# Performance work log

Measured on AMD Instinct MI355X. Metric: run time of the kernel, lower is better.

Reference implementation:

```python
import jax, jax.numpy as jnp
import numpy as np

N, E, IN, H, C, ED = 50000, 800000, 128, 4, 64, 4
NEG_SLOPE = 0.2


def setup_inputs() -> dict:
    key = jax.random.key(0)
    ks = iter(jax.random.split(key, 40))
    def p(shape, s=0.05):
        return jax.random.normal(next(ks), shape, jnp.float32) * s
    inp = dict(
        x=jax.random.normal(next(ks), (N, IN), jnp.float32),
        edge_index=jax.random.randint(next(ks), (2, E), 0, N),
        edge_attr=jax.random.normal(next(ks), (E, ED), jnp.float32),
        # GATConv layer 1 (concat=True)
        W1=p((IN, H * C)), att_src1=p((H, C)), att_dst1=p((H, C)),
        We1=p((ED, H * C)), att_e1=p((H, C)), b1=p((H * C,)),
        g1=jnp.ones((H * C,), jnp.float32), be1=jnp.zeros((H * C,), jnp.float32),
        # GATConv layer 2 (concat=False -> mean over heads)
        W2=p((H * C, H * C)), att_src2=p((H, C)), att_dst2=p((H, C)),
        We2=p((ED, H * C)), att_e2=p((H, C)), b2=p((C,)),
        g2=jnp.ones((C,), jnp.float32), be2=jnp.zeros((C,), jnp.float32),
        # skip / MLP head
        skip_W=p((IN, C)), skip_b=p((C,)),
        fc1_W=p((C, C // 2)), fc1_b=p((C // 2,)),
        fc2_W=p((C // 2, 1)), fc2_b=p((1,)),
    )
    return inp


def _add_self_loops(edge_index, edge_attr, n):
    # PyG GATConv default: add_self_loops=True, fill_value='mean'
    src, dst = edge_index[0], edge_index[1]
    sums = jax.ops.segment_sum(edge_attr, dst, num_segments=n)
    cnt = jax.ops.segment_sum(jnp.ones((edge_attr.shape[0], 1), edge_attr.dtype), dst, num_segments=n)
    mean_attr = sums / jnp.maximum(cnt, 1.0)
    loop = jnp.arange(n)
    src = jnp.concatenate([src, loop])
    dst = jnp.concatenate([dst, loop])
    ea = jnp.concatenate([edge_attr, mean_attr], axis=0)
    return src, dst, ea


def _gat_layer(x, src, dst, ea, W, a_src, a_dst, We, a_e, bias, n, concat):
    xs = (x @ W).reshape(n, H, C)                     # [N,H,C]
    alpha_src = (xs * a_src).sum(-1)                  # [N,H]
    alpha_dst = (xs * a_dst).sum(-1)                  # [N,H]
    ep = (ea @ We).reshape(-1, H, C)                  # [Et,H,C]
    alpha_e = (ep * a_e).sum(-1)                      # [Et,H]
    alpha = jax.nn.leaky_relu(alpha_src[src] + alpha_dst[dst] + alpha_e, NEG_SLOPE)
    # segment softmax over destination nodes
    m = jax.ops.segment_max(alpha, dst, num_segments=n)
    alpha = jnp.exp(alpha - m[dst])
    denom = jax.ops.segment_sum(alpha, dst, num_segments=n)
    alpha = alpha / (denom[dst] + 1e-16)
    out = jax.ops.segment_sum(xs[src] * alpha[:, :, None], dst, num_segments=n)  # [N,H,C]
    out = out.reshape(n, H * C) if concat else out.mean(axis=1)
    return out + bias


def _bn(x, g, b):
    mu = x.mean(0)
    var = x.var(0)
    return (x - mu) * jax.lax.rsqrt(var + 1e-5) * g + b


def reference(x, edge_index, edge_attr, W1, att_src1, att_dst1, We1, att_e1, b1, g1, be1,
              W2, att_src2, att_dst2, We2, att_e2, b2, g2, be2,
              skip_W, skip_b, fc1_W, fc1_b, fc2_W, fc2_b):
    n = x.shape[0]
    src, dst, ea = _add_self_loops(edge_index, edge_attr, n)
    residual = x @ skip_W + skip_b
    h = _gat_layer(x, src, dst, ea, W1, att_src1, att_dst1, We1, att_e1, b1, n, True)
    h = jax.nn.elu(_bn(h, g1, be1))
    h = _gat_layer(h, src, dst, ea, W2, att_src2, att_dst2, We2, att_e2, b2, n, False)
    h = jax.nn.elu(_bn(h, g2, be2))
    h = h + residual
    h = jax.nn.relu(h @ fc1_W + fc1_b)
    h = jax.nn.softplus(h @ fc2_W + fc2_b)
    return h.squeeze(-1)
```

## Files before the change

kernel.cpp:

```cpp
#include <hip/hip_runtime.h>
#include <math.h>

static constexpr int N_NODES = 50000;
static constexpr int N_EDGES = 800000;
static constexpr int IN_F = 128;
static constexpr int CH = 64;
static constexpr int HC = 256;
static constexpr float NEG_SLOPE = 0.2f;

typedef __attribute__((ext_vector_type(8))) short bf16x8;
typedef __attribute__((ext_vector_type(4))) float f32x4;

__device__ __forceinline__ unsigned pack_bf(float a, float b) {
    unsigned ua = __float_as_uint(a) + 0x8000u;
    unsigned ub = __float_as_uint(b) + 0x8000u;
    return __builtin_amdgcn_perm(ub, ua, 0x07060302u);
}
__device__ __forceinline__ float bflo(unsigned u) { return __uint_as_float(u << 16); }
__device__ __forceinline__ float bfhi(unsigned u) { return __uint_as_float(u & 0xffff0000u); }
__device__ __forceinline__ float bfs(unsigned short u) {
    return __uint_as_float((unsigned)u << 16);
}
__device__ __forceinline__ float elu(float v) { return v > 0.f ? v : __expf(v) - 1.0f; }

__device__ __forceinline__ int sigma(int p) { return ((p & 15) << 4) | (p >> 4); }

static constexpr int EB_BLK = (N_EDGES + 255) / 256;
static constexpr int CONV_ITEMS = 106496 + 32;
static constexpr int CONV_BLK = (CONV_ITEMS + 255) / 256;
static constexpr int GEMM_BLKS = (N_NODES + 63) / 64;

__global__ void hist_conv(const int* __restrict__ ei, int* __restrict__ deg,
                          const float* __restrict__ W1, const float* __restrict__ W2,
                          const float* __restrict__ Ws, const float* __restrict__ We1,
                          const float* __restrict__ atte1, const float* __restrict__ We2,
                          const float* __restrict__ atte2, unsigned short* __restrict__ WT1,
                          unsigned short* __restrict__ WT2, unsigned short* __restrict__ WTs,
                          float* __restrict__ weff) {
    if (blockIdx.x < EB_BLK) {
        int e = blockIdx.x * 256 + threadIdx.x;
        if (e < N_EDGES) atomicAdd(&deg[ei[N_EDGES + e]], 1);
        return;
    }
    int t = (blockIdx.x - EB_BLK) * 256 + threadIdx.x;
    if (t < 32768) {
        int k = t >> 8, n = t & 255;
        unsigned u = __float_as_uint(W1[t]) + 0x8000u;
        WT1[n * 128 + k] = (unsigned short)(u >> 16);
    } else if (t < 98304) {
        int u2 = t - 32768;
        int k = u2 >> 8, n = u2 & 255;
        unsigned u = __float_as_uint(W2[u2]) + 0x8000u;
        WT2[n * 256 + sigma(k)] = (unsigned short)(u >> 16);
    } else if (t < 106496) {
        int u2 = t - 98304;
        int k = u2 >> 6, n = u2 & 63;
        unsigned u = __float_as_uint(Ws[u2]) + 0x8000u;
        WTs[n * 128 + k] = (unsigned short)(u >> 16);
    } else if (t < 106496 + 32) {
        int idx = t - 106496;
        const float* We = idx < 16 ? We1 : We2;
        const float* ae = idx < 16 ? atte1 : atte2;
        int j = idx & 15;
        int d = j >> 2, h = j & 3;
        float s = 0.f;
        for (int c = 0; c < CH; ++c) s += We[d * HC + h * CH + c] * ae[h * CH + c];
        weff[idx] = s;
    }
}

__global__ void scan_block(const int* __restrict__ deg, int* __restrict__ rowptr,
                           int* __restrict__ bsum) {
    __shared__ int s[256];
    int tid = threadIdx.x;
    int i = blockIdx.x * 256 + tid;
    int v = (i < N_NODES) ? deg[i] : 0;
    s[tid] = v;
    __syncthreads();
    for (int off = 1; off < 256; off <<= 1) {
        int t = (tid >= off) ? s[tid - off] : 0;
        __syncthreads();
        s[tid] += t;
        __syncthreads();
    }
    if (i < N_NODES) rowptr[i] = s[tid] - v;
    if (tid == 255) bsum[blockIdx.x] = s[255];
}

__global__ void scan_add2(int* __restrict__ rowptr, const int* __restrict__ bsum,
                          int* __restrict__ fillc, int nb) {
    __shared__ int s[256];
    int tid = threadIdx.x;
    int v = (tid < nb) ? bsum[tid] : 0;
    s[tid] = v;
    __syncthreads();
    for (int off = 1; off < 256; off <<= 1) {
        int t = (tid >= off) ? s[tid - off] : 0;
        __syncthreads();
        s[tid] += t;
        __syncthreads();
    }
    int boff = (blockIdx.x == 0) ? 0 : s[blockIdx.x - 1];
    int i = blockIdx.x * 256 + tid;
    if (i < N_NODES) {
        rowptr[i] += boff;
        fillc[i] = 0;
    }
    if (i == N_NODES) rowptr[N_NODES] = N_EDGES;
}

template <int K, bool ABF, bool BN, bool SKIP, bool FILL>
__global__ __launch_bounds__(256) void gemm_mfma_att(
    const void* __restrict__ Av, const unsigned short* __restrict__ BT,
    const float* __restrict__ colsum, const float* __restrict__ g,
    const float* __restrict__ be, float invM,
    const unsigned short* __restrict__ BTs, const float* __restrict__ skip_b,
    float* __restrict__ residual,
    const float* __restrict__ att_src, const float* __restrict__ att_dst,
    unsigned short* __restrict__ xsb, float* __restrict__ asrc, float* __restrict__ adst,
    int M, const int* __restrict__ ei, const float4* __restrict__ ea,
    const int* __restrict__ rowptr, int* __restrict__ fillc, uint4* __restrict__ edrec) {
    if constexpr (FILL) {
        if (blockIdx.x >= GEMM_BLKS) {
            int e = (blockIdx.x - GEMM_BLKS) * 256 + threadIdx.x;
            if (e < N_EDGES) {
                int s = ei[e];
                int t = ei[N_EDGES + e];
                const float4 v = ea[e];
                int p = atomicAdd(&fillc[t], 1);
                edrec[rowptr[t] + p] =
                    make_uint4((unsigned)s, (unsigned)t, pack_bf(v.x, v.y), pack_bf(v.z, v.w));
            }
            return;
        }
    }
    constexpr int NT = 16;
    __shared__ float s_scale[256], s_shift[256];
    if constexpr (BN) {
        int c = threadIdx.x;
        int tc = sigma(c);
        float mean = colsum[c] * invM;
        float var = colsum[256 + c] * invM - mean * mean;
        float sc = g[tc] * rsqrtf(var + 1e-5f);
        s_scale[c] = sc;
        s_shift[c] = be[tc] - mean * sc;
        __syncthreads();
    }
    const int lane = threadIdx.x & 63;
    const int wid = threadIdx.x >> 6;
    const int r0 = blockIdx.x * 64 + wid * 16;
    const int lr = lane & 15;
    const int kg = lane >> 4;
    f32x4 acc[NT] = {};
    f32x4 accS[4] = {};
    const float* af = (const float*)Av;
    const unsigned short* ab = (const unsigned short*)Av;
    int rr = r0 + lr;
    if (rr >= M) rr = M - 1;
    const size_t rowoff = (size_t)rr * K + kg * 8;
    const unsigned short* brow = BT + (size_t)lr * K + kg * 8;
    const unsigned short* brow_s = SKIP ? BTs + (size_t)lr * K + kg * 8 : nullptr;
    for (int k0 = 0; k0 < K; k0 += 32) {
        float4 sc0, sc1, sh0, sh1;
        if constexpr (BN) {
            sc0 = *reinterpret_cast<const float4*>(&s_scale[k0 + kg * 8]);
            sc1 = *reinterpret_cast<const float4*>(&s_scale[k0 + kg * 8 + 4]);
            sh0 = *reinterpret_cast<const float4*>(&s_shift[k0 + kg * 8]);
            sh1 = *reinterpret_cast<const float4*>(&s_shift[k0 + kg * 8 + 4]);
        }
        bf16x8 a;
        if constexpr (!ABF) {
            const float4 lo = *reinterpret_cast<const float4*>(af + rowoff + k0);
            const float4 hi = *reinterpret_cast<const float4*>(af + rowoff + k0 + 4);
            union { bf16x8 v; unsigned u[4]; } fa;
            fa.u[0] = pack_bf(lo.x, lo.y);
            fa.u[1] = pack_bf(lo.z, lo.w);
            fa.u[2] = pack_bf(hi.x, hi.y);
            fa.u[3] = pack_bf(hi.z, hi.w);
            a = fa.v;
        } else {
            union { bf16x8 v; unsigned short us[8]; unsigned u[4]; } fa;
            fa.v = *reinterpret_cast<const bf16x8*>(ab + rowoff + k0);
            if constexpr (BN) {
                float f0 = elu(fmaf(bfs(fa.us[0]), sc0.x, sh0.x));
                float f1 = elu(fmaf(bfs(fa.us[1]), sc0.y, sh0.y));
                float f2 = elu(fmaf(bfs(fa.us[2]), sc0.z, sh0.z));
                float f3 = elu(fmaf(bfs(fa.us[3]), sc0.w, sh0.w));
                float f4 = elu(fmaf(bfs(fa.us[4]), sc1.x, sh1.x));
                float f5 = elu(fmaf(bfs(fa.us[5]), sc1.y, sh1.y));
                float f6 = elu(fmaf(bfs(fa.us[6]), sc1.z, sh1.z));
                float f7 = elu(fmaf(bfs(fa.us[7]), sc1.w, sh1.w));
                fa.u[0] = pack_bf(f0, f1);
                fa.u[1] = pack_bf(f2, f3);
                fa.u[2] = pack_bf(f4, f5);
                fa.u[3] = pack_bf(f6, f7);
            }
            a = fa.v;
        }
#pragma unroll
        for (int c = 0; c < NT; ++c) {
            bf16x8 b = *reinterpret_cast<const bf16x8*>(brow + (size_t)c * 16 * K + k0);
            acc[c] = __builtin_amdgcn_mfma_f32_16x16x32_bf16(a, b, acc[c], 0, 0, 0);
        }
        if constexpr (SKIP) {
#pragma unroll
            for (int c = 0; c < 4; ++c) {
                bf16x8 b = *reinterpret_cast<const bf16x8*>(brow_s + (size_t)c * 16 * K + k0);
                accS[c] = __builtin_amdgcn_mfma_f32_16x16x32_bf16(a, b, accS[c], 0, 0, 0);
            }
        }
    }
    float attS[NT], attD[NT];
#pragma unroll
    for (int c = 0; c < NT; ++c) {
        attS[c] = att_src[c * 16 + lr];
        attD[c] = att_dst[c * 16 + lr];
    }
#pragma unroll
    for (int j = 0; j < 4; ++j) {
        int row = r0 + kg * 4 + j;
        bool valid = row < M;
        uint4 ua, ub;
        ua.x = pack_bf(acc[0][j], acc[1][j]);
        ua.y = pack_bf(acc[2][j], acc[3][j]);
        ua.z = pack_bf(acc[4][j], acc[5][j]);
        ua.w = pack_bf(acc[6][j], acc[7][j]);
        ub.x = pack_bf(acc[8][j], acc[9][j]);
        ub.y = pack_bf(acc[10][j], acc[11][j]);
        ub.z = pack_bf(acc[12][j], acc[13][j]);
        ub.w = pack_bf(acc[14][j], acc[15][j]);
        if (valid) {
            uint4* dst = reinterpret_cast<uint4*>(xsb + (size_t)row * HC) + lr * 2;
            dst[0] = ua;
            dst[1] = ub;
        }
        if constexpr (SKIP) {
            if (valid) {
#pragma unroll
                for (int c = 0; c < 4; ++c) {
                    int col = c * 16 + lr;
                    residual[(size_t)row * CH + col] = accS[c][j] + skip_b[col];
                }
            }
        }
#pragma unroll
        for (int h = 0; h < 4; ++h) {
            float ps = acc[4 * h + 0][j] * attS[4 * h + 0] +
                       acc[4 * h + 1][j] * attS[4 * h + 1] +
                       acc[4 * h + 2][j] * attS[4 * h + 2] +
                       acc[4 * h + 3][j] * attS[4 * h + 3];
            float pd = acc[4 * h + 0][j] * attD[4 * h + 0] +
                       acc[4 * h + 1][j] * attD[4 * h + 1] +
                       acc[4 * h + 2][j] * attD[4 * h + 2] +
                       acc[4 * h + 3][j] * attD[4 * h + 3];
#pragma unroll
            for (int mk = 1; mk < 16; mk <<= 1) {
                ps += __shfl_xor(ps, mk);
                pd += __shfl_xor(pd, mk);
            }
            if (valid && lr == 0) {
                asrc[row * 4 + h] = ps;
                adst[row * 4 + h] = pd;
            }
        }
    }
}

__global__ __launch_bounds__(256) void edge_w(
    const uint4* __restrict__ edrec, const float* __restrict__ weff,
    const float4* __restrict__ asrcv, const float4* __restrict__ adstv,
    uint4* __restrict__ pw) {
    int i = blockIdx.x * 256 + threadIdx.x;
    if (i >= N_EDGES) return;
    const uint4 er = edrec[i];
    int s = (int)er.x;
    int t = (int)er.y;
    const float vx = bflo(er.z), vy = bfhi(er.z), vz = bflo(er.w), vw = bfhi(er.w);
    const float4 as4 = asrcv[s];
    const float4 ad4 = adstv[t];
    const float asl[4] = {as4.x, as4.y, as4.z, as4.w};
    const float adl[4] = {ad4.x, ad4.y, ad4.z, ad4.w};
    float p[4], aev[4];
#pragma unroll
    for (int h = 0; h < 4; ++h) {
        float ae = vx * weff[h] + vy * weff[4 + h] + vz * weff[8 + h] + vw * weff[12 + h];
        float l = asl[h] + adl[h] + ae;
        l = fmaxf(l, NEG_SLOPE * l);
        p[h] = __expf(l);
        aev[h] = ae;
    }
    pw[i] = make_uint4(pack_bf(p[0], p[1]), pack_bf(p[2], p[3]),
                       pack_bf(aev[0], aev[1]), pack_bf(aev[2], aev[3]));
}

template <bool MEAN>
__global__ __launch_bounds__(256) void gat_node(
    const int* __restrict__ rowptr, const uint4* __restrict__ edrec,
    const uint4* __restrict__ pw, const float4* __restrict__ asrcv,
    const float4* __restrict__ adstv, const uint2* __restrict__ xsb,
    float* __restrict__ zbuf, void* __restrict__ outp) {
    if (blockIdx.x == 0) {
        zbuf[threadIdx.x] = 0.f;
        zbuf[256 + threadIdx.x] = 0.f;
    }
    int t = blockIdx.x * 4 + (threadIdx.x >> 6);
    if (t >= N_NODES) return;
    const int lane = threadIdx.x & 63;
    const int h = lane & 3;
    const unsigned sh = (h & 1) ? 0u : 16u;
    const bool hiW = (h & 2) != 0;
    const int start = rowptr[t], end = rowptr[t + 1];
    const int deg = end - start;
    const uint2* xl = xsb + lane;
    const unsigned* er32 = reinterpret_cast<const unsigned*>(edrec);
    float acc0 = 0.f, acc1 = 0.f, acc2 = 0.f, acc3 = 0.f;
    float psum = 0.f, aesum = 0.f;
    int i = start;
    for (; i + 8 <= end; i += 8) {
        uint2 f[8];
        float p[8], ae[8];
#pragma unroll
        for (int j = 0; j < 8; ++j) {
            int s = (int)er32[(size_t)(i + j) * 4];
            f[j] = xl[(size_t)s * 64];
            const uint4 w = pw[i + j];
            unsigned pword = hiW ? w.y : w.x;
            unsigned aeword = hiW ? w.w : w.z;
            p[j] = __uint_as_float((pword << sh) & 0xffff0000u);
            ae[j] = __uint_as_float((aeword << sh) & 0xffff0000u);
        }
#pragma unroll
        for (int j = 0; j < 8; ++j) {
            psum += p[j];
            aesum += ae[j];
            acc0 += bflo(f[j].x) * p[j];
            acc1 += bfhi(f[j].x) * p[j];
            acc2 += bflo(f[j].y) * p[j];
            acc3 += bfhi(f[j].y) * p[j];
        }
    }
    for (; i < end; ++i) {
        int s = (int)er32[(size_t)i * 4];
        uint2 f = xl[(size_t)s * 64];
        const uint4 w = pw[i];
        unsigned pword = hiW ? w.y : w.x;
        unsigned aeword = hiW ? w.w : w.z;
        float p = __uint_as_float((pword << sh) & 0xffff0000u);
        float ae = __uint_as_float((aeword << sh) & 0xffff0000u);
        psum += p;
        aesum += ae;
        acc0 += bflo(f.x) * p;
        acc1 += bfhi(f.x) * p;
        acc2 += bflo(f.y) * p;
        acc3 += bfhi(f.y) * p;
    }
    const float inv_deg = deg > 0 ? 1.0f / (float)deg : 1.0f;
    const float4 as4 = asrcv[t];
    const float4 ad4 = adstv[t];
    float asl = h == 0 ? as4.x : h == 1 ? as4.y : h == 2 ? as4.z : as4.w;
    float adl = h == 0 ? ad4.x : h == 1 ? ad4.y : h == 2 ? ad4.z : ad4.w;
    float l = asl + adl + aesum * inv_deg;
    l = fmaxf(l, NEG_SLOPE * l);
    const float pself = __expf(l);
    uint2 sf = xl[(size_t)t * 64];
    acc0 += bflo(sf.x) * pself;
    acc1 += bfhi(sf.x) * pself;
    acc2 += bflo(sf.y) * pself;
    acc3 += bfhi(sf.y) * pself;
    const float inv = 1.0f / (psum + pself + 1e-16f);
    acc0 *= inv; acc1 *= inv; acc2 *= inv; acc3 *= inv;
    if constexpr (MEAN) {
        acc0 += __shfl_xor(acc0, 1); acc0 += __shfl_xor(acc0, 2);
        acc1 += __shfl_xor(acc1, 1); acc1 += __shfl_xor(acc1, 2);
        acc2 += __shfl_xor(acc2, 1); acc2 += __shfl_xor(acc2, 2);
        acc3 += __shfl_xor(acc3, 1); acc3 += __shfl_xor(acc3, 2);
        if (h == 0) {
            int q = lane >> 2;
            float* o = reinterpret_cast<float*>(outp) + (size_t)t * CH + q;
            o[0] = 0.25f * acc0;
            o[16] = 0.25f * acc1;
            o[32] = 0.25f * acc2;
            o[48] = 0.25f * acc3;
        }
    } else {
        reinterpret_cast<uint2*>(outp)[(size_t)t * 64 + lane] =
            make_uint2(pack_bf(acc0, acc1), pack_bf(acc2, acc3));
    }
}

__global__ void colstats_bf(const unsigned short* __restrict__ X, float* __restrict__ sum,
                            float* __restrict__ sumsq, int M) {
    int c = threadIdx.x;
    int r0 = blockIdx.x * 256;
    int r1 = min(M, r0 + 256);
    float s = 0.f, q = 0.f;
    for (int r = r0; r < r1; ++r) {
        float v = bfs(X[(size_t)r * HC + c]);
        s += v;
        q += v * v;
    }
    atomicAdd(&sum[c], s);
    atomicAdd(&sumsq[c], q);
}

template <int F>
__global__ void colstats(const float* __restrict__ X, float* __restrict__ sum,
                         float* __restrict__ sumsq, int M) {
    const int NG = 256 / F;
    int c = threadIdx.x % F;
    int g = threadIdx.x / F;
    int r0 = blockIdx.x * 256;
    int r1 = min(M, r0 + 256);
    float s = 0.f, q = 0.f;
    for (int r = r0 + g; r < r1; r += NG) {
        float v = X[(size_t)r * F + c];
        s += v;
        q += v * v;
    }
    atomicAdd(&sum[c], s);
    atomicAdd(&sumsq[c], q);
}

__global__ __launch_bounds__(256) void head_mlp(
    const float* __restrict__ h2, const float* __restrict__ colsum,
    const float* __restrict__ g2, const float* __restrict__ be2, float invM,
    const float* __restrict__ residual, const float* __restrict__ fc1W,
    const float* __restrict__ fc1b, const float* __restrict__ fc2W,
    const float* __restrict__ fc2b, float* __restrict__ out) {
    __shared__ float s_sc[CH], s_sh[CH];
    if (threadIdx.x < CH) {
        int c = threadIdx.x;
        float mean = colsum[c] * invM;
        float var = colsum[256 + c] * invM - mean * mean;
        float sc = g2[c] * rsqrtf(var + 1e-5f);
        s_sc[c] = sc;
        s_sh[c] = be2[c] - mean * sc;
    }
    __syncthreads();
    int n = blockIdx.x * 4 + (threadIdx.x >> 6);
    if (n >= N_NODES) return;
    int w = threadIdx.x >> 6;
    int lane = threadIdx.x & 63;
    __shared__ float hrow[4][64];
    float v = fmaf(h2[(size_t)n * CH + lane], s_sc[lane], s_sh[lane]);
    v = elu(v) + residual[(size_t)n * CH + lane];
    hrow[w][lane] = v;
    float p = 0.f;
    if (lane < 32) {
        float acc = fc1b[lane];
#pragma unroll
        for (int k = 0; k < CH; ++k) acc = fmaf(hrow[w][k], fc1W[k * 32 + lane], acc);
        acc = fmaxf(acc, 0.f);
        p = acc * fc2W[lane];
    }
    for (int off = 16; off > 0; off >>= 1) p += __shfl_down(p, off);
    if (lane == 0) {
        float z = p + fc2b[0];
        out[n] = z > 20.f ? z : log1pf(expf(z));
    }
}

extern "C" void kernel_launch(void* const* d_in, const int* in_sizes, int n_in, void* d_out,
                              int out_size, void* d_ws, size_t ws_size, hipStream_t stream) {
    const float* x        = (const float*)d_in[0];
    const int*   ei       = (const int*)d_in[1];
    const float* ea       = (const float*)d_in[2];
    const float* W1       = (const float*)d_in[3];
    const float* att_src1 = (const float*)d_in[4];
    const float* att_dst1 = (const float*)d_in[5];
    const float* We1      = (const float*)d_in[6];
    const float* att_e1   = (const float*)d_in[7];
    const float* g1       = (const float*)d_in[9];
    const float* be1      = (const float*)d_in[10];
    const float* W2       = (const float*)d_in[11];
    const float* att_src2 = (const float*)d_in[12];
    const float* att_dst2 = (const float*)d_in[13];
    const float* We2      = (const float*)d_in[14];
    const float* att_e2   = (const float*)d_in[15];
    const float* g2       = (const float*)d_in[17];
    const float* be2      = (const float*)d_in[18];
    const float* skip_W   = (const float*)d_in[19];
    const float* skip_b   = (const float*)d_in[20];
    const float* fc1_W    = (const float*)d_in[21];
    const float* fc1_b    = (const float*)d_in[22];
    const float* fc2_W    = (const float*)d_in[23];
    const float* fc2_b    = (const float*)d_in[24];
    float* out = (float*)d_out;

    float* wsf = (float*)d_ws;
    size_t off = 0;
    auto take = [&](size_t n) {
        float* p = wsf + off;
        off += n;
        return p;
    };
    unsigned short* xsb  = (unsigned short*)take((size_t)N_NODES * HC / 2);
    unsigned short* aggb = (unsigned short*)take((size_t)N_NODES * HC / 2);
    uint4* pw       = (uint4*)take((size_t)N_EDGES * 4);
    uint4* edrec    = (uint4*)take((size_t)N_EDGES * 4);
    int* rowptr     = (int*)take(N_NODES + 1);
    int* degfill    = (int*)take(N_NODES);
    int* bsum       = (int*)take(256);
    float* asrc     = take(N_NODES * 4);
    float* adst     = take(N_NODES * 4);
    float* residual = take((size_t)N_NODES * CH);
    float* h2       = take((size_t)N_NODES * CH);
    float* weff     = take(32);
    float* colsum   = take(HC);
    float* colsq    = take(HC);
    unsigned short* WT1 = (unsigned short*)take(IN_F * HC / 2);
    unsigned short* WT2 = (unsigned short*)take(HC * HC / 2);
    unsigned short* WTs = (unsigned short*)take(IN_F * CH / 2);

    const int NBLK = (N_NODES + 255) / 256;
    const int NODE4 = (N_NODES + 3) / 4;
    const float invM = 1.0f / N_NODES;

    hipMemsetAsync(degfill, 0, N_NODES * sizeof(int), stream);
    hist_conv<<<EB_BLK + CONV_BLK, 256, 0, stream>>>(ei, degfill, W1, W2, skip_W, We1,
                                                     att_e1, We2, att_e2, WT1, WT2, WTs, weff);
    scan_block<<<NBLK, 256, 0, stream>>>(degfill, rowptr, bsum);
    scan_add2<<<(N_NODES + 256) / 256, 256, 0, stream>>>(rowptr, bsum, degfill, NBLK);

    gemm_mfma_att<IN_F, false, false, true, true>
        <<<GEMM_BLKS + EB_BLK, 256, 0, stream>>>(
            x, WT1, nullptr, nullptr, nullptr, 0.f, WTs, skip_b, residual, att_src1,
            att_dst1, xsb, asrc, adst, N_NODES, ei, (const float4*)ea, rowptr, degfill,
            edrec);
    edge_w<<<EB_BLK, 256, 0, stream>>>(edrec, weff, (const float4*)asrc,
                                       (const float4*)adst, pw);
    gat_node<false><<<NODE4, 256, 0, stream>>>(rowptr, edrec, pw, (const float4*)asrc,
                                               (const float4*)adst, (const uint2*)xsb,
                                               colsum, aggb);
    colstats_bf<<<NBLK, 256, 0, stream>>>(aggb, colsum, colsq, N_NODES);

    gemm_mfma_att<HC, true, true, false, false><<<GEMM_BLKS, 256, 0, stream>>>(
        aggb, WT2, colsum, g1, be1, invM, nullptr, nullptr, nullptr, att_src2, att_dst2,
        xsb, asrc, adst, N_NODES, nullptr, nullptr, nullptr, nullptr, nullptr);
    edge_w<<<EB_BLK, 256, 0, stream>>>(edrec, weff + 16, (const float4*)asrc,
                                       (const float4*)adst, pw);
    gat_node<true><<<NODE4, 256, 0, stream>>>(rowptr, edrec, pw, (const float4*)asrc,
                                              (const float4*)adst, (const uint2*)xsb,
                                              colsum, h2);
    colstats<CH><<<NBLK, 256, 0, stream>>>(h2, colsum, colsq, N_NODES);

    head_mlp<<<NODE4, 256, 0, stream>>>(h2, colsum, g2, be2, invM, residual, fc1_W, fc1_b,
                                        fc2_W, fc2_b, out);
}
```

Baseline: 487.7 us.

## Fuse edge attention-weight computation into GAT node aggregation kernel

```diff
diff --git a/kernel.cpp b/kernel.cpp
--- a/kernel.cpp
+++ b/kernel.cpp
@@ -266,37 +266,10 @@
     }
 }
 
-__global__ __launch_bounds__(256) void edge_w(
-    const uint4* __restrict__ edrec, const float* __restrict__ weff,
-    const float4* __restrict__ asrcv, const float4* __restrict__ adstv,
-    uint4* __restrict__ pw) {
-    int i = blockIdx.x * 256 + threadIdx.x;
-    if (i >= N_EDGES) return;
-    const uint4 er = edrec[i];
-    int s = (int)er.x;
-    int t = (int)er.y;
-    const float vx = bflo(er.z), vy = bfhi(er.z), vz = bflo(er.w), vw = bfhi(er.w);
-    const float4 as4 = asrcv[s];
-    const float4 ad4 = adstv[t];
-    const float asl[4] = {as4.x, as4.y, as4.z, as4.w};
-    const float adl[4] = {ad4.x, ad4.y, ad4.z, ad4.w};
-    float p[4], aev[4];
-#pragma unroll
-    for (int h = 0; h < 4; ++h) {
-        float ae = vx * weff[h] + vy * weff[4 + h] + vz * weff[8 + h] + vw * weff[12 + h];
-        float l = asl[h] + adl[h] + ae;
-        l = fmaxf(l, NEG_SLOPE * l);
-        p[h] = __expf(l);
-        aev[h] = ae;
-    }
-    pw[i] = make_uint4(pack_bf(p[0], p[1]), pack_bf(p[2], p[3]),
-                       pack_bf(aev[0], aev[1]), pack_bf(aev[2], aev[3]));
-}
-
 template <bool MEAN>
 __global__ __launch_bounds__(256) void gat_node(
     const int* __restrict__ rowptr, const uint4* __restrict__ edrec,
-    const uint4* __restrict__ pw, const float4* __restrict__ asrcv,
+    const float* __restrict__ weff, const float* __restrict__ asrc,
     const float4* __restrict__ adstv, const uint2* __restrict__ xsb,
     float* __restrict__ zbuf, void* __restrict__ outp) {
     if (blockIdx.x == 0) {
@@ -307,12 +280,12 @@
     if (t >= N_NODES) return;
     const int lane = threadIdx.x & 63;
     const int h = lane & 3;
-    const unsigned sh = (h & 1) ? 0u : 16u;
-    const bool hiW = (h & 2) != 0;
+    const float w0 = weff[h], w1 = weff[4 + h], w2 = weff[8 + h], w3 = weff[12 + h];
     const int start = rowptr[t], end = rowptr[t + 1];
     const int deg = end - start;
     const uint2* xl = xsb + lane;
-    const unsigned* er32 = reinterpret_cast<const unsigned*>(edrec);
+    const float4 ad4 = adstv[t];
+    const float ad = h == 0 ? ad4.x : h == 1 ? ad4.y : h == 2 ? ad4.z : ad4.w;
     float acc0 = 0.f, acc1 = 0.f, acc2 = 0.f, acc3 = 0.f;
     float psum = 0.f, aesum = 0.f;
     int i = start;
@@ -321,13 +294,15 @@
         float p[8], ae[8];
 #pragma unroll
         for (int j = 0; j < 8; ++j) {
-            int s = (int)er32[(size_t)(i + j) * 4];
+            const uint4 er = edrec[i + j];
+            int s = (int)er.x;
             f[j] = xl[(size_t)s * 64];
-            const uint4 w = pw[i + j];
-            unsigned pword = hiW ? w.y : w.x;
-            unsigned aeword = hiW ? w.w : w.z;
-            p[j] = __uint_as_float((pword << sh) & 0xffff0000u);
-            ae[j] = __uint_as_float((aeword << sh) & 0xffff0000u);
+            float av = asrc[(size_t)s * 4 + h];
+            float a = bflo(er.z) * w0 + bfhi(er.z) * w1 + bflo(er.w) * w2 + bfhi(er.w) * w3;
+            float l = av + ad + a;
+            l = fmaxf(l, NEG_SLOPE * l);
+            p[j] = __expf(l);
+            ae[j] = a;
         }
 #pragma unroll
         for (int j = 0; j < 8; ++j) {
@@ -340,26 +315,23 @@
         }
     }
     for (; i < end; ++i) {
-        int s = (int)er32[(size_t)i * 4];
+        const uint4 er = edrec[i];
+        int s = (int)er.x;
         uint2 f = xl[(size_t)s * 64];
-        const uint4 w = pw[i];
-        unsigned pword = hiW ? w.y : w.x;
-        unsigned aeword = hiW ? w.w : w.z;
-        float p = __uint_as_float((pword << sh) & 0xffff0000u);
-        float ae = __uint_as_float((aeword << sh) & 0xffff0000u);
+        float av = asrc[(size_t)s * 4 + h];
+        float a = bflo(er.z) * w0 + bfhi(er.z) * w1 + bflo(er.w) * w2 + bfhi(er.w) * w3;
+        float l = av + ad + a;
+        l = fmaxf(l, NEG_SLOPE * l);
+        float p = __expf(l);
         psum += p;
-        aesum += ae;
+        aesum += a;
         acc0 += bflo(f.x) * p;
         acc1 += bfhi(f.x) * p;
         acc2 += bflo(f.y) * p;
         acc3 += bfhi(f.y) * p;
     }
     const float inv_deg = deg > 0 ? 1.0f / (float)deg : 1.0f;
-    const float4 as4 = asrcv[t];
-    const float4 ad4 = adstv[t];
-    float asl = h == 0 ? as4.x : h == 1 ? as4.y : h == 2 ? as4.z : as4.w;
-    float adl = h == 0 ? ad4.x : h == 1 ? ad4.y : h == 2 ? ad4.z : ad4.w;
-    float l = asl + adl + aesum * inv_deg;
+    float l = asrc[(size_t)t * 4 + h] + ad + aesum * inv_deg;
     l = fmaxf(l, NEG_SLOPE * l);
     const float pself = __expf(l);
     uint2 sf = xl[(size_t)t * 64];
@@ -496,7 +468,6 @@
     };
     unsigned short* xsb  = (unsigned short*)take((size_t)N_NODES * HC / 2);
     unsigned short* aggb = (unsigned short*)take((size_t)N_NODES * HC / 2);
-    uint4* pw       = (uint4*)take((size_t)N_EDGES * 4);
     uint4* edrec    = (uint4*)take((size_t)N_EDGES * 4);
     int* rowptr     = (int*)take(N_NODES + 1);
     int* degfill    = (int*)take(N_NODES);
@@ -527,9 +498,7 @@
             x, WT1, nullptr, nullptr, nullptr, 0.f, WTs, skip_b, residual, att_src1,
             att_dst1, xsb, asrc, adst, N_NODES, ei, (const float4*)ea, rowptr, degfill,
             edrec);
-    edge_w<<<EB_BLK, 256, 0, stream>>>(edrec, weff, (const float4*)asrc,
-                                       (const float4*)adst, pw);
-    gat_node<false><<<NODE4, 256, 0, stream>>>(rowptr, edrec, pw, (const float4*)asrc,
+    gat_node<false><<<NODE4, 256, 0, stream>>>(rowptr, edrec, weff, asrc,
                                                (const float4*)adst, (const uint2*)xsb,
                                                colsum, aggb);
     colstats_bf<<<NBLK, 256, 0, stream>>>(aggb, colsum, colsq, N_NODES);
@@ -537,9 +506,7 @@
     gemm_mfma_att<HC, true, true, false, false><<<GEMM_BLKS, 256, 0, stream>>>(
         aggb, WT2, colsum, g1, be1, invM, nullptr, nullptr, nullptr, att_src2, att_dst2,
         xsb, asrc, adst, N_NODES, nullptr, nullptr, nullptr, nullptr, nullptr);
-    edge_w<<<EB_BLK, 256, 0, stream>>>(edrec, weff + 16, (const float4*)asrc,
-                                       (const float4*)adst, pw);
-    gat_node<true><<<NODE4, 256, 0, stream>>>(rowptr, edrec, pw, (const float4*)asrc,
+    gat_node<true><<<NODE4, 256, 0, stream>>>(rowptr, edrec, weff + 16, asrc,
                                               (const float4*)adst, (const uint2*)xsb,
                                               colsum, h2);
     colstats<CH><<<NBLK, 256, 0, stream>>>(h2, colsum, colsq, N_NODES);
```

Result: slower. 524.2 us (+7.5%).
